# Optimization experiments

Hardware: AMD Instinct MI355X
Metric: run time of the kernel (lower is better)

## Reference

```python
import jax, jax.numpy as jnp
import numpy as np

NEG_SLOPE = 0.1
LN_EPS = 1e-5


def setup_inputs() -> dict:
    key = jax.random.key(0)
    ks = jax.random.split(key, 8)
    B, S, IN, OUT, H = 16, 1024, 512, 512, 8
    DH = OUT // H
    x = jax.random.normal(ks[0], (B, S, IN), dtype=jnp.float32)
    scale = 1.0 / np.sqrt(IN)
    # per-head projection weights, stored as [H, in, dh] so y = x @ W
    wq = jax.random.uniform(ks[1], (H, IN, DH), minval=-scale, maxval=scale, dtype=jnp.float32)
    wk = jax.random.uniform(ks[2], (H, IN, DH), minval=-scale, maxval=scale, dtype=jnp.float32)
    wv = jax.random.uniform(ks[3], (H, IN, DH), minval=-scale, maxval=scale, dtype=jnp.float32)
    scale_o = 1.0 / np.sqrt(OUT)
    w_out = jax.random.uniform(ks[4], (OUT, OUT), minval=-scale_o, maxval=scale_o, dtype=jnp.float32)
    b_out = jax.random.uniform(ks[5], (OUT,), minval=-scale_o, maxval=scale_o, dtype=jnp.float32)
    ln_gamma = jnp.ones((OUT,), dtype=jnp.float32)
    ln_beta = jnp.zeros((OUT,), dtype=jnp.float32)
    return {"x": x, "wq": wq, "wk": wk, "wv": wv, "w_out": w_out,
            "b_out": b_out, "ln_gamma": ln_gamma, "ln_beta": ln_beta}


def reference(x, wq, wk, wv, w_out, b_out, ln_gamma, ln_beta):
    B, S, _ = x.shape
    H, _, DH = wq.shape
    # per-head projections, vectorized over heads: [H, B, S, DH]
    q = jnp.einsum('bsf,hfd->hbsd', x, wq)
    k = jnp.einsum('bsf,hfd->hbsd', x, wk)
    v = jnp.einsum('bsf,hfd->hbsd', x, wv)
    # attention scores [H, B, S, S]
    att = jnp.einsum('hbsd,hbtd->hbst', q, k) / jnp.sqrt(jnp.float32(DH))
    # FAITHFUL to source: softmax over dim=0 of the per-head [B,S,S] tensor,
    # i.e. the BATCH axis (axis=1 in our [H,B,S,S] layout)
    att = jax.nn.softmax(att, axis=1)
    out = jnp.einsum('hbst,hbtd->hbsd', att, v)
    # concat heads -> [B, S, H*DH]
    heads_cat = jnp.transpose(out, (1, 2, 0, 3)).reshape(B, S, H * DH)
    y = heads_cat @ w_out + b_out
    # LayerNorm over last dim
    mu = jnp.mean(y, axis=-1, keepdims=True)
    var = jnp.var(y, axis=-1, keepdims=True)
    y = (y - mu) * jax.lax.rsqrt(var + LN_EPS) * ln_gamma + ln_beta
    # LeakyReLU(0.1)
    return jnp.where(y >= 0, y, NEG_SLOPE * y)
```

## Files before the change

kernel.cpp:

```cpp
#include <hip/hip_runtime.h>

typedef unsigned short u16;
typedef unsigned int uint;
typedef __attribute__((ext_vector_type(8))) short bf16x8;
typedef __attribute__((ext_vector_type(4))) float f32x4;

#define NBATCH 16
#define SDIM   1024
#define INDIM  512
#define OUTDIM 512
#define HEADS  8
#define DHEAD  64
#define MROWS  (NBATCH * SDIM)
#define KDIM   512
#define QSCALE (0.125f * 1.44269504088896340736f)

__device__ __forceinline__ u16 f2bf(float f) {
  union { float f; uint u; } v; v.f = f;
  uint u = v.u;
  return (u16)((u + 0x7FFFu + ((u >> 16) & 1u)) >> 16);
}

__device__ __forceinline__ uint pkbf(float a, float b) {
  return (uint)f2bf(a) | ((uint)f2bf(b) << 16);
}

__device__ __forceinline__ uint pkbf_fast(float a, float b) {
  union { float f; uint u; } ua, ub; ua.f = a; ub.f = b;
  return __builtin_amdgcn_perm(ub.u + 0x8000u, ua.u + 0x8000u, 0x07060302);
}

__device__ __forceinline__ float bf2f(u16 v) {
  union { uint u; float f; } c; c.u = (uint)v << 16;
  return c.f;
}

__device__ __forceinline__ void gload16(const void* g, void* l) {
  __builtin_amdgcn_global_load_lds(
      (const __attribute__((address_space(1))) uint*)g,
      (__attribute__((address_space(3))) uint*)l, 16, 0, 0);
}

__global__ __launch_bounds__(256) void prep_kernel(
    const float* __restrict__ x, const float* __restrict__ wq,
    const float* __restrict__ wk, const float* __restrict__ wv,
    const float* __restrict__ w_out,
    u16* __restrict__ xb, u16* __restrict__ W1T, u16* __restrict__ W2T) {
  __shared__ float T[64 * 65];
  const int tid = threadIdx.x;
  if (blockIdx.x < 2048) {
    const int NX4 = MROWS * INDIM / 4;
    int stride = 2048 * 256;
    for (int i = blockIdx.x * 256 + tid; i < NX4; i += stride) {
      float4 v = ((const float4*)x)[i];
      ((ushort4*)xb)[i] = make_ushort4(f2bf(v.x), f2bf(v.y), f2bf(v.z), f2bf(v.w));
    }
    return;
  }
  const int t = blockIdx.x - 2048;
  const int rr = tid >> 6, cc = tid & 63;
  if (t < 192) {
    int proj = t >> 6, h = (t >> 3) & 7, f0 = (t & 7) * 64;
    const float* src = (proj == 0) ? wq : (proj == 1) ? wk : wv;
    float scale = (proj == 0) ? QSCALE : 1.0f;
    for (int it = 0; it < 16; it++) {
      int fi = it * 4 + rr;
      T[fi * 65 + cc] = src[((size_t)h * 512 + f0 + fi) * 64 + cc] * scale;
    }
    __syncthreads();
    u16* dst = W1T + ((size_t)(proj * 512 + h * 64)) * 512 + f0;
    for (int it = 0; it < 16; it++) {
      int d = it * 4 + rr;
      dst[(size_t)d * 512 + cc] = f2bf(T[cc * 65 + d]);
    }
  } else {
    int t2 = t - 192;
    int n0 = (t2 >> 3) * 64, f0 = (t2 & 7) * 64;
    for (int it = 0; it < 16; it++) {
      int fi = it * 4 + rr;
      T[fi * 65 + cc] = w_out[(size_t)(f0 + fi) * 512 + n0 + cc];
    }
    __syncthreads();
    for (int it = 0; it < 16; it++) {
      int ni = it * 4 + rr;
      W2T[(size_t)(n0 + ni) * 512 + f0 + cc] = f2bf(T[cc * 65 + ni]);
    }
  }
}

template <int EPI>
__global__ __launch_bounds__(256) void gemm128(
    const u16* __restrict__ A, const u16* __restrict__ Bt,
    u16* __restrict__ Qb, u16* __restrict__ Kb, u16* __restrict__ VTb,
    u16* __restrict__ Yb) {
  __shared__ u16 As[128 * 32];
  __shared__ u16 Bs[128 * 32];
  const int tid = threadIdx.x;
  const int w = tid >> 6, lane = tid & 63;
  const int quad = lane >> 4, ln = lane & 15;
  const int wm = w >> 1, wn = w & 1;
  const int m0 = blockIdx.y * 128, n0 = blockIdx.x * 128;

  f32x4 zero4 = {0.f, 0.f, 0.f, 0.f};
  f32x4 acc[4][4];
  for (int i = 0; i < 4; i++)
    for (int j = 0; j < 4; j++) acc[i][j] = zero4;

  const char* Ag = (const char*)(A + (size_t)m0 * KDIM);
  const char* Bg = (const char*)(Bt + (size_t)n0 * KDIM);
  const int r0 = w * 16 + (lane >> 2);
  const int cb = (lane & 3) * 16;

  for (int kk = 0; kk < KDIM; kk += 32) {
    __syncthreads();
    gload16(Ag + (size_t)r0 * (KDIM * 2) + kk * 2 + cb, (char*)As + w * 1024);
    gload16(Ag + (size_t)(r0 + 64) * (KDIM * 2) + kk * 2 + cb, (char*)As + 4096 + w * 1024);
    gload16(Bg + (size_t)r0 * (KDIM * 2) + kk * 2 + cb, (char*)Bs + w * 1024);
    gload16(Bg + (size_t)(r0 + 64) * (KDIM * 2) + kk * 2 + cb, (char*)Bs + 4096 + w * 1024);
    __syncthreads();
    bf16x8 af[4], bfr[4];
    for (int mt = 0; mt < 4; mt++)
      af[mt] = *(const bf16x8*)&As[(wm * 64 + mt * 16 + ln) * 32 + quad * 8];
    for (int nt = 0; nt < 4; nt++)
      bfr[nt] = *(const bf16x8*)&Bs[(wn * 64 + nt * 16 + ln) * 32 + quad * 8];
    for (int mt = 0; mt < 4; mt++)
      for (int nt = 0; nt < 4; nt++)
        acc[mt][nt] = __builtin_amdgcn_mfma_f32_16x16x32_bf16(af[mt], bfr[nt], acc[mt][nt], 0, 0, 0);
  }

  for (int mt = 0; mt < 4; mt++) {
    int mbase = m0 + wm * 64 + mt * 16 + quad * 4;
    int b = mbase >> 10, sbase = mbase & 1023;
    for (int nt = 0; nt < 4; nt++) {
      f32x4 c = acc[mt][nt];
      int col = n0 + wn * 64 + nt * 16 + ln;
      if (EPI == 0) {
        int proj = n0 >> 9;
        int hd = col & 511, h = hd >> 6, d = hd & 63;
        if (proj == 2) {
          *(ushort4*)&VTb[((size_t)(h * 16 + b) * 64 + d) * 1024 + sbase] =
              make_ushort4(f2bf(c[0]), f2bf(c[1]), f2bf(c[2]), f2bf(c[3]));
        } else {
          u16* dst = (proj == 0) ? Qb : Kb;
          size_t base = ((size_t)(h * 16 + b) * 1024) * 64 + d;
          dst[base + (size_t)(sbase + 0) * 64] = f2bf(c[0]);
          dst[base + (size_t)(sbase + 1) * 64] = f2bf(c[1]);
          dst[base + (size_t)(sbase + 2) * 64] = f2bf(c[2]);
          dst[base + (size_t)(sbase + 3) * 64] = f2bf(c[3]);
        }
      } else {
        Yb[(size_t)(mbase + 0) * OUTDIM + col] = f2bf(c[0]);
        Yb[(size_t)(mbase + 1) * OUTDIM + col] = f2bf(c[1]);
        Yb[(size_t)(mbase + 2) * OUTDIM + col] = f2bf(c[2]);
        Yb[(size_t)(mbase + 3) * OUTDIM + col] = f2bf(c[3]);
      }
    }
  }
}

__global__ __launch_bounds__(512, 4) void attnA_kernel(
    const u16* __restrict__ Qb, const u16* __restrict__ Kb,
    u16* __restrict__ LinvX) {
  __shared__ u16 Qt[2 * 64 * 64];
  __shared__ u16 Kt[2 * 256 * 64];
  const int tid = threadIdx.x;
  const int w = tid >> 6, lane = tid & 63;
  const int quad = lane >> 4, ln = lane & 15;
  const int ws = w & 3, wt = w >> 2;
  const int h = blockIdx.x & 7;
  const int s0 = ((blockIdx.x >> 3) & 15) * 64;
  const int tq = blockIdx.x >> 7;
  const int t0 = tq * 256;
  const int srow = tid >> 3, sseg = tid & 7;

  const u16* Qh = Qb + (size_t)h * 16 * 65536;
  const u16* Kh = Kb + (size_t)h * 16 * 65536;

  f32x4 zero4 = {0.f, 0.f, 0.f, 0.f};
  f32x4 Lacc[8];
  for (int i = 0; i < 8; i++) Lacc[i] = zero4;

  {
    gload16(Qh + (size_t)(s0 + srow) * 64 + sseg * 8, (char*)Qt + w * 1024);
    const u16* Kg = Kh + (size_t)(t0 + srow) * 64 + sseg * 8;
    gload16(Kg,            (char*)Kt + w * 1024);
    gload16(Kg + 64 * 64,  (char*)Kt + 8192 + w * 1024);
    gload16(Kg + 128 * 64, (char*)Kt + 16384 + w * 1024);
    gload16(Kg + 192 * 64, (char*)Kt + 24576 + w * 1024);
  }

  for (int b = 0; b < 16; b++) {
    const int cur = b & 1;
    __syncthreads();
    if (b < 15) {
      const u16* Qg = Qh + (size_t)(b + 1) * 65536 + (size_t)(s0 + srow) * 64 + sseg * 8;
      const u16* Kg = Kh + (size_t)(b + 1) * 65536 + (size_t)(t0 + srow) * 64 + sseg * 8;
      char* Kd = (char*)Kt + (cur ^ 1) * 32768 + w * 1024;
      gload16(Qg, (char*)Qt + (cur ^ 1) * 8192 + w * 1024);
      gload16(Kg,            Kd);
      gload16(Kg + 64 * 64,  Kd + 8192);
      gload16(Kg + 128 * 64, Kd + 16384);
      gload16(Kg + 192 * 64, Kd + 24576);
    }
    const u16* Qr = &Qt[cur * 4096 + (ws * 16 + ln) * 64];
    bf16x8 q0 = *(const bf16x8*)&Qr[quad * 8];
    bf16x8 q1 = *(const bf16x8*)&Qr[32 + quad * 8];
    for (int tsub = 0; tsub < 8; tsub++) {
      const u16* Kr = &Kt[cur * 16384 + (wt * 128 + tsub * 16 + ln) * 64];
      f32x4 cc = zero4;
      cc = __builtin_amdgcn_mfma_f32_16x16x32_bf16(*(const bf16x8*)&Kr[quad * 8], q0, cc, 0, 0, 0);
      cc = __builtin_amdgcn_mfma_f32_16x16x32_bf16(*(const bf16x8*)&Kr[32 + quad * 8], q1, cc, 0, 0, 0);
      f32x4 L = Lacc[tsub];
      L[0] += __builtin_amdgcn_exp2f(cc[0]); L[1] += __builtin_amdgcn_exp2f(cc[1]);
      L[2] += __builtin_amdgcn_exp2f(cc[2]); L[3] += __builtin_amdgcn_exp2f(cc[3]);
      Lacc[tsub] = L;
    }
  }

  const int sg = s0 + ws * 16 + ln;
  for (int tsub = 0; tsub < 8; tsub++) {
    const int tc = tq * 16 + wt * 8 + tsub;
    f32x4 L = Lacc[tsub];
    uint2 pk = make_uint2(
        pkbf(__builtin_amdgcn_rcpf(L[0]), __builtin_amdgcn_rcpf(L[1])),
        pkbf(__builtin_amdgcn_rcpf(L[2]), __builtin_amdgcn_rcpf(L[3])));
    *(uint2*)&LinvX[(((size_t)(h * 64 + tc)) * 1024 + sg) * 16 + quad * 4] = pk;
  }
}

__global__ __launch_bounds__(256, 4) void attnB_kernel(
    const u16* __restrict__ Qb, const u16* __restrict__ Kb,
    const u16* __restrict__ VTb, const u16* __restrict__ LinvX,
    u16* __restrict__ hc) {
  __shared__ u16 Ks[2 * 32 * 64];
  __shared__ u16 Vs[2 * 64 * 32];
  __shared__ u16 Pp[4 * 2 * 16 * 40];
  const int tid = threadIdx.x;
  const int w = tid >> 6, lane = tid & 63;
  const int quad = lane >> 4, ln = lane & 15;
  const int h = blockIdx.x & 7, b = (blockIdx.x >> 3) & 15, sblk = blockIdx.x >> 7;
  const int ss0 = sblk * 128 + w * 32;
  const int krow = tid >> 3;
  const int ksw = ((tid & 7) ^ (krow & 7)) * 8;
  const int vrow = tid >> 2;
  const int vsw = ((tid & 3) ^ ((tid >> 3) & 3)) * 8;

  const u16* Kbase = Kb + (size_t)(h * 16 + b) * 65536;
  const u16* Vbase = VTb + (size_t)(h * 16 + b) * 65536;
  const u16* LinvH = LinvX + (size_t)h * 64 * 1024 * 16;

  f32x4 zero4 = {0.f, 0.f, 0.f, 0.f};
  bf16x8 qf[2][2];
  for (int a = 0; a < 2; a++) {
    const u16* Qp = Qb + ((size_t)(h * 16 + b) * 1024 + ss0 + a * 16 + ln) * 64;
    qf[a][0] = *(const bf16x8*)&Qp[quad * 8];
    qf[a][1] = *(const bf16x8*)&Qp[32 + quad * 8];
  }
  f32x4 o[2][4];
  for (int a = 0; a < 2; a++)
    for (int df = 0; df < 4; df++) o[a][df] = zero4;

  gload16(Kbase + (size_t)krow * 64 + ksw, (char*)Ks + w * 1024);
  gload16(Vbase + (size_t)vrow * 1024 + vsw, (char*)Vs + w * 1024);

  const int fsw = (quad ^ (ln & 7)) * 8;
  const int vfsw = (quad ^ ((ln >> 1) & 3)) * 8;

  for (int it = 0; it < 32; ++it) {
    const int cur = it & 1;
    const int t0 = it * 32;
    __syncthreads();
    if (it < 31) {
      gload16(Kbase + (size_t)(t0 + 32 + krow) * 64 + ksw,
              (char*)Ks + (cur ^ 1) * 4096 + w * 1024);
      gload16(Vbase + (size_t)vrow * 1024 + t0 + 32 + vsw,
              (char*)Vs + (cur ^ 1) * 4096 + w * 1024);
    }
    bf16x8 kf[2][2], vf[4];
    for (int tsub = 0; tsub < 2; tsub++) {
      const u16* Kr = &Ks[cur * 2048 + (tsub * 16 + ln) * 64];
      kf[tsub][0] = *(const bf16x8*)&Kr[fsw];
      kf[tsub][1] = *(const bf16x8*)&Kr[fsw ^ 32];
    }
    for (int df = 0; df < 4; df++)
      vf[df] = *(const bf16x8*)&Vs[cur * 2048 + (df * 16 + ln) * 32 + vfsw];

    for (int a = 0; a < 2; a++) {
      for (int tsub = 0; tsub < 2; tsub++) {
        const int tc = it * 2 + tsub;
        ushort4 lin = *(const ushort4*)&LinvH[
            (((size_t)tc) * 1024 + ss0 + a * 16 + ln) * 16 + quad * 4];
        f32x4 cc = zero4;
        cc = __builtin_amdgcn_mfma_f32_16x16x32_bf16(kf[tsub][0], qf[a][0], cc, 0, 0, 0);
        cc = __builtin_amdgcn_mfma_f32_16x16x32_bf16(kf[tsub][1], qf[a][1], cc, 0, 0, 0);
        float p0 = __builtin_amdgcn_exp2f(cc[0]) * bf2f(lin.x);
        float p1 = __builtin_amdgcn_exp2f(cc[1]) * bf2f(lin.y);
        float p2 = __builtin_amdgcn_exp2f(cc[2]) * bf2f(lin.z);
        float p3 = __builtin_amdgcn_exp2f(cc[3]) * bf2f(lin.w);
        uint2 pk = make_uint2(pkbf_fast(p0, p1), pkbf_fast(p2, p3));
        *(uint2*)&Pp[(w * 2 + a) * 640 + ln * 40 + tsub * 16 + quad * 4] = pk;
      }
      bf16x8 pa = *(const bf16x8*)&Pp[(w * 2 + a) * 640 + ln * 40 + quad * 8];
      for (int df = 0; df < 4; df++)
        o[a][df] = __builtin_amdgcn_mfma_f32_16x16x32_bf16(pa, vf[df], o[a][df], 0, 0, 0);
    }
  }

  for (int a = 0; a < 2; a++) {
    for (int df = 0; df < 4; df++) {
      f32x4 c = o[a][df];
      for (int r = 0; r < 4; r++) {
        int sg = ss0 + a * 16 + quad * 4 + r;
        hc[((size_t)(b * 1024 + sg)) * 512 + h * 64 + df * 16 + ln] = f2bf(c[r]);
      }
    }
  }
}

__global__ __launch_bounds__(256) void ln_kernel(
    const u16* __restrict__ Yb, const float* __restrict__ b_out,
    const float* __restrict__ gamma, const float* __restrict__ beta,
    float* __restrict__ out) {
  const int w = threadIdx.x >> 6, lane = threadIdx.x & 63;
  const int row = blockIdx.x * 4 + w;
  ushort4 ya = *(const ushort4*)&Yb[(size_t)row * 512 + lane * 8];
  ushort4 yc = *(const ushort4*)&Yb[(size_t)row * 512 + lane * 8 + 4];
  float4 b0 = ((const float4*)b_out)[lane * 2], b1 = ((const float4*)b_out)[lane * 2 + 1];
  float v[8];
  v[0] = bf2f(ya.x) + b0.x; v[1] = bf2f(ya.y) + b0.y;
  v[2] = bf2f(ya.z) + b0.z; v[3] = bf2f(ya.w) + b0.w;
  v[4] = bf2f(yc.x) + b1.x; v[5] = bf2f(yc.y) + b1.y;
  v[6] = bf2f(yc.z) + b1.z; v[7] = bf2f(yc.w) + b1.w;
  float s = 0.f, s2 = 0.f;
  for (int j = 0; j < 8; j++) { s += v[j]; s2 += v[j] * v[j]; }
  for (int off = 32; off; off >>= 1) {
    s += __shfl_xor(s, off);
    s2 += __shfl_xor(s2, off);
  }
  float mean = s * (1.0f / 512.0f);
  float var = s2 * (1.0f / 512.0f) - mean * mean;
  float rs = rsqrtf(var + 1e-5f);
  float4 g0 = ((const float4*)gamma)[lane * 2], g1 = ((const float4*)gamma)[lane * 2 + 1];
  float4 e0 = ((const float4*)beta)[lane * 2], e1 = ((const float4*)beta)[lane * 2 + 1];
  float g[8] = {g0.x, g0.y, g0.z, g0.w, g1.x, g1.y, g1.z, g1.w};
  float e[8] = {e0.x, e0.y, e0.z, e0.w, e1.x, e1.y, e1.z, e1.w};
  float r[8];
  for (int j = 0; j < 8; j++) {
    float y = (v[j] - mean) * rs * g[j] + e[j];
    r[j] = y >= 0.f ? y : 0.1f * y;
  }
  float4 o0 = make_float4(r[0], r[1], r[2], r[3]);
  float4 o1 = make_float4(r[4], r[5], r[6], r[7]);
  ((float4*)out)[(size_t)row * 128 + lane * 2] = o0;
  ((float4*)out)[(size_t)row * 128 + lane * 2 + 1] = o1;
}

extern "C" void kernel_launch(void* const* d_in, const int* in_sizes, int n_in,
                              void* d_out, int out_size, void* d_ws, size_t ws_size,
                              hipStream_t stream) {
  const float* x      = (const float*)d_in[0];
  const float* wq     = (const float*)d_in[1];
  const float* wk     = (const float*)d_in[2];
  const float* wv     = (const float*)d_in[3];
  const float* w_out  = (const float*)d_in[4];
  const float* b_out  = (const float*)d_in[5];
  const float* gamma  = (const float*)d_in[6];
  const float* beta   = (const float*)d_in[7];
  float* out = (float*)d_out;

  char* ws = (char*)d_ws;
  size_t off = 0;
  u16* xb  = (u16*)(ws + off); off += (size_t)MROWS * INDIM * 2;
  u16* W1T = (u16*)(ws + off); off += (size_t)3 * OUTDIM * INDIM * 2;
  u16* W2T = (u16*)(ws + off); off += (size_t)OUTDIM * INDIM * 2;
  u16* Qb  = (u16*)(ws + off); off += (size_t)HEADS * NBATCH * SDIM * DHEAD * 2;
  u16* Kb  = (u16*)(ws + off); off += (size_t)HEADS * NBATCH * SDIM * DHEAD * 2;
  u16* VTb = (u16*)(ws + off); off += (size_t)HEADS * NBATCH * SDIM * DHEAD * 2;
  u16* hc  = (u16*)(ws + off); off += (size_t)MROWS * OUTDIM * 2;
  u16* LinvX = (u16*)(ws + off);
  u16* Yb = LinvX;

  prep_kernel<<<2304, 256, 0, stream>>>(x, wq, wk, wv, w_out, xb, W1T, W2T);
  gemm128<0><<<dim3(12, 128), 256, 0, stream>>>(xb, W1T, Qb, Kb, VTb, nullptr);
  attnA_kernel<<<512, 512, 0, stream>>>(Qb, Kb, LinvX);
  attnB_kernel<<<1024, 256, 0, stream>>>(Qb, Kb, VTb, LinvX, hc);
  gemm128<1><<<dim3(4, 128), 256, 0, stream>>>(hc, W2T, nullptr, nullptr, nullptr, Yb);
  ln_kernel<<<4096, 256, 0, stream>>>(Yb, b_out, gamma, beta, out);
}
```

Baseline: 249.5 us.

## Double-buffer GEMM LDS tiles and stage epilogue through LDS for vector stores

The bf16 GEMM used for the QKV and output projections now loads the next K-slice into an alternate LDS buffer while computing on the current one, which drops one barrier per iteration and overlaps global loads with MFMA work. The epilogue writes accumulators into a per-wave LDS tile (transposed for the V^T output) and then issues 16-byte coalesced global stores instead of scattered 2-byte stores. LDS use grows to 32KB per block, which may lower occupancy.

```diff
diff --git a/kernel.cpp b/kernel.cpp
--- a/kernel.cpp
+++ b/kernel.cpp
@@ -93,8 +93,7 @@
     const u16* __restrict__ A, const u16* __restrict__ Bt,
     u16* __restrict__ Qb, u16* __restrict__ Kb, u16* __restrict__ VTb,
     u16* __restrict__ Yb) {
-  __shared__ u16 As[128 * 32];
-  __shared__ u16 Bs[128 * 32];
+  __shared__ u16 lds[16384];
   const int tid = threadIdx.x;
   const int w = tid >> 6, lane = tid & 63;
   const int quad = lane >> 4, ln = lane & 15;
@@ -111,48 +110,81 @@
   const int r0 = w * 16 + (lane >> 2);
   const int cb = (lane & 3) * 16;
 
-  for (int kk = 0; kk < KDIM; kk += 32) {
+  {
+    const char* Ak = Ag + (size_t)r0 * 1024 + cb;
+    const char* Bk = Bg + (size_t)r0 * 1024 + cb;
+    gload16(Ak,             (char*)lds + w * 1024);
+    gload16(Ak + 64 * 1024, (char*)lds + 4096 + w * 1024);
+    gload16(Bk,             (char*)lds + 16384 + w * 1024);
+    gload16(Bk + 64 * 1024, (char*)lds + 16384 + 4096 + w * 1024);
+  }
+
+  for (int kk = 0; kk < 16; kk++) {
+    const int cur = kk & 1;
     __syncthreads();
-    gload16(Ag + (size_t)r0 * (KDIM * 2) + kk * 2 + cb, (char*)As + w * 1024);
-    gload16(Ag + (size_t)(r0 + 64) * (KDIM * 2) + kk * 2 + cb, (char*)As + 4096 + w * 1024);
-    gload16(Bg + (size_t)r0 * (KDIM * 2) + kk * 2 + cb, (char*)Bs + w * 1024);
-    gload16(Bg + (size_t)(r0 + 64) * (KDIM * 2) + kk * 2 + cb, (char*)Bs + 4096 + w * 1024);
-    __syncthreads();
+    if (kk < 15) {
+      const char* Ak = Ag + (size_t)r0 * 1024 + (kk + 1) * 64 + cb;
+      const char* Bk = Bg + (size_t)r0 * 1024 + (kk + 1) * 64 + cb;
+      char* Ad = (char*)lds + (cur ^ 1) * 8192 + w * 1024;
+      char* Bd = (char*)lds + 16384 + (cur ^ 1) * 8192 + w * 1024;
+      gload16(Ak,             Ad);
+      gload16(Ak + 64 * 1024, Ad + 4096);
+      gload16(Bk,             Bd);
+      gload16(Bk + 64 * 1024, Bd + 4096);
+    }
     bf16x8 af[4], bfr[4];
     for (int mt = 0; mt < 4; mt++)
-      af[mt] = *(const bf16x8*)&As[(wm * 64 + mt * 16 + ln) * 32 + quad * 8];
+      af[mt] = *(const bf16x8*)&lds[cur * 4096 + (wm * 64 + mt * 16 + ln) * 32 + quad * 8];
     for (int nt = 0; nt < 4; nt++)
-      bfr[nt] = *(const bf16x8*)&Bs[(wn * 64 + nt * 16 + ln) * 32 + quad * 8];
+      bfr[nt] = *(const bf16x8*)&lds[8192 + cur * 4096 + (wn * 64 + nt * 16 + ln) * 32 + quad * 8];
     for (int mt = 0; mt < 4; mt++)
       for (int nt = 0; nt < 4; nt++)
         acc[mt][nt] = __builtin_amdgcn_mfma_f32_16x16x32_bf16(af[mt], bfr[nt], acc[mt][nt], 0, 0, 0);
   }
 
-  for (int mt = 0; mt < 4; mt++) {
-    int mbase = m0 + wm * 64 + mt * 16 + quad * 4;
-    int b = mbase >> 10, sbase = mbase & 1023;
-    for (int nt = 0; nt < 4; nt++) {
-      f32x4 c = acc[mt][nt];
-      int col = n0 + wn * 64 + nt * 16 + ln;
-      if (EPI == 0) {
-        int proj = n0 >> 9;
-        int hd = col & 511, h = hd >> 6, d = hd & 63;
-        if (proj == 2) {
-          *(ushort4*)&VTb[((size_t)(h * 16 + b) * 64 + d) * 1024 + sbase] =
-              make_ushort4(f2bf(c[0]), f2bf(c[1]), f2bf(c[2]), f2bf(c[3]));
-        } else {
-          u16* dst = (proj == 0) ? Qb : Kb;
-          size_t base = ((size_t)(h * 16 + b) * 1024) * 64 + d;
-          dst[base + (size_t)(sbase + 0) * 64] = f2bf(c[0]);
-          dst[base + (size_t)(sbase + 1) * 64] = f2bf(c[1]);
-          dst[base + (size_t)(sbase + 2) * 64] = f2bf(c[2]);
-          dst[base + (size_t)(sbase + 3) * 64] = f2bf(c[3]);
-        }
-      } else {
-        Yb[(size_t)(mbase + 0) * OUTDIM + col] = f2bf(c[0]);
-        Yb[(size_t)(mbase + 1) * OUTDIM + col] = f2bf(c[1]);
-        Yb[(size_t)(mbase + 2) * OUTDIM + col] = f2bf(c[2]);
-        Yb[(size_t)(mbase + 3) * OUTDIM + col] = f2bf(c[3]);
+  __syncthreads();
+  u16* Tw = lds + w * 4096;
+  const int colbase = n0 + wn * 64;
+  const int rowbase = m0 + wm * 64;
+  const int proj = (EPI == 0) ? (colbase >> 9) : -1;
+  if (EPI == 0 && proj == 2) {
+    for (int mt = 0; mt < 4; mt++)
+      for (int nt = 0; nt < 4; nt++) {
+        f32x4 c = acc[mt][nt];
+        for (int r = 0; r < 4; r++)
+          Tw[(nt * 16 + ln) * 64 + mt * 16 + quad * 4 + r] = f2bf(c[r]);
+      }
+  } else {
+    for (int mt = 0; mt < 4; mt++)
+      for (int nt = 0; nt < 4; nt++) {
+        f32x4 c = acc[mt][nt];
+        for (int r = 0; r < 4; r++)
+          Tw[(mt * 16 + quad * 4 + r) * 64 + nt * 16 + ln] = f2bf(c[r]);
+      }
+  }
+  const int trow = lane >> 3;
+  const int tcol = (lane & 7) * 8;
+  if (EPI == 1) {
+    u16* dst = Yb + (size_t)rowbase * OUTDIM + colbase + tcol;
+    for (int i = 0; i < 8; i++) {
+      uint4 v = *(const uint4*)&Tw[(i * 8 + trow) * 64 + tcol];
+      *(uint4*)&dst[(size_t)(i * 8 + trow) * OUTDIM] = v;
+    }
+  } else {
+    const int hd = colbase & 511, h = hd >> 6;
+    const int b = rowbase >> 10, sb = rowbase & 1023;
+    if (proj == 2) {
+      u16* dst = VTb + (size_t)(h * 16 + b) * 65536 + sb + tcol;
+      for (int i = 0; i < 8; i++) {
+        uint4 v = *(const uint4*)&Tw[(i * 8 + trow) * 64 + tcol];
+        *(uint4*)&dst[(size_t)(i * 8 + trow) * 1024] = v;
+      }
+    } else {
+      u16* dst = (proj == 0 ? Qb : Kb) +
+                 (size_t)(h * 16 + b) * 65536 + (size_t)sb * 64 + tcol;
+      for (int i = 0; i < 8; i++) {
+        uint4 v = *(const uint4*)&Tw[(i * 8 + trow) * 64 + tcol];
+        *(uint4*)&dst[(size_t)(i * 8 + trow) * 64] = v;
       }
     }
   }
```

Result: slower. 264.7 us (+6.1%).
